# Performance work log

Hardware: AMD Instinct MI355X
Metric: run time of the kernel (lower is better)

Reference implementation:

```python
import jax, jax.numpy as jnp
import numpy as np

RANK = 16
ALPHA = 32
SCALING = ALPHA / RANK  # alpha / rank


def setup_inputs() -> dict:
    key = jax.random.key(0)
    k_x, k_w, k_b, k_a, k_bb = jax.random.split(key, 5)
    B, S, D_IN, D_OUT = 4, 2048, 4096, 4096
    x = jax.random.normal(k_x, (B, S, D_IN), dtype=jnp.float32)
    W = jax.random.normal(k_w, (D_OUT, D_IN), dtype=jnp.float32) * (1.0 / np.sqrt(D_IN))
    b = jax.random.normal(k_b, (D_OUT,), dtype=jnp.float32) * 0.02
    # LoRA init: A ~ N(0, 2/rank); B is zeros in the module, but we use small
    # random values so the adapter path is numerically exercised.
    lora_A = jax.random.normal(k_a, (RANK, D_IN), dtype=jnp.float32) * np.sqrt(2.0 / RANK)
    lora_B = jax.random.normal(k_bb, (D_OUT, RANK), dtype=jnp.float32) * 0.02
    return {"x": x, "W": W, "b": b, "lora_A": lora_A, "lora_B": lora_B}


def reference(x, W, b, lora_A, lora_B):
    # Base linear: x @ W^T + b
    base = jnp.einsum("bsd,od->bso", x, W) + b
    # LoRA path, fused as two rank-r matmuls (never materializing B@A):
    # (x @ A^T) @ B^T * scaling  ==  F.linear(x, B@A) * scaling
    xa = jnp.einsum("bsd,rd->bsr", x, lora_A)      # [B,S,r]
    lora = jnp.einsum("bsr,or->bso", xa, lora_B)    # [B,S,D_out]
    return base + lora * SCALING
```

## Files before the change

kernel.cpp:

```cpp
#include <hip/hip_runtime.h>
#include <hip/hip_bf16.h>

#define K_DIM 4096
#define N_DIM 4096
#define R_DIM 16
#define SCALING_F 2.0f

#define BM 256
#define BN 256
#define BK 64

typedef __attribute__((ext_vector_type(8))) short bf16x8;
typedef __attribute__((ext_vector_type(4))) float f32x4;

__device__ __forceinline__ ushort f2bf(float f) {
  union { float f; unsigned u; } v; v.f = f;
  unsigned u = v.u;
  u += 0x7FFF + ((u >> 16) & 1);
  return (ushort)(u >> 16);
}

__global__ void convert_x_kernel(const float* __restrict__ x,
                                 ushort* __restrict__ xb, long n4) {
  long i = (long)blockIdx.x * blockDim.x + threadIdx.x;
  long stride = (long)gridDim.x * blockDim.x;
  for (; i < n4; i += stride) {
    long idx = i * 4;
    float4 v = *(const float4*)(x + idx);
    ushort4 o;
    o.x = f2bf(v.x); o.y = f2bf(v.y); o.z = f2bf(v.z); o.w = f2bf(v.w);
    *(ushort4*)(xb + idx) = o;
  }
}

__global__ void fold_w_kernel(const float* __restrict__ W,
                              const float* __restrict__ A,
                              const float* __restrict__ Bl,
                              ushort* __restrict__ wb) {
  int o = blockIdx.x;
  float breg[R_DIM];
#pragma unroll
  for (int r = 0; r < R_DIM; ++r) breg[r] = Bl[o * R_DIM + r] * SCALING_F;
  for (int d0 = threadIdx.x * 4; d0 < K_DIM; d0 += blockDim.x * 4) {
    float4 w = *(const float4*)(W + (size_t)o * K_DIM + d0);
    float a0 = w.x, a1 = w.y, a2 = w.z, a3 = w.w;
#pragma unroll
    for (int r = 0; r < R_DIM; ++r) {
      float4 a = *(const float4*)(A + (size_t)r * K_DIM + d0);
      a0 += breg[r] * a.x; a1 += breg[r] * a.y;
      a2 += breg[r] * a.z; a3 += breg[r] * a.w;
    }
    ushort4 ob;
    ob.x = f2bf(a0); ob.y = f2bf(a1); ob.z = f2bf(a2); ob.w = f2bf(a3);
    *(ushort4*)(wb + (size_t)o * K_DIM + d0) = ob;
  }
}


#define RS 8192L

#define GLOAD(SRC, LOFF)                                                    \
  __builtin_amdgcn_global_load_lds(                                         \
      (const __attribute__((address_space(1))) void*)(SRC),                 \
      (__attribute__((address_space(3))) void*)(smem + (LOFF)), 16, 0, 0)

#define LDSA(BUF) ((BUF) * 32768)
#define LDSB(BUF) (65536 + (BUF) * 32768)

#define ST_A_EVEN(T, BUF) do {                                              \
    GLOAD(aS + (size_t)(T) * 128,            LDSA(BUF) + ldsDst);           \
    GLOAD(aS + (size_t)(T) * 128 + 128 * RS, LDSA(BUF) + 16384 + ldsDst); } while (0)
#define ST_A_ODD(T, BUF) do {                                               \
    GLOAD(aS + (size_t)(T) * 128 + 64 * RS,  LDSA(BUF) + 8192 + ldsDst);    \
    GLOAD(aS + (size_t)(T) * 128 + 192 * RS, LDSA(BUF) + 24576 + ldsDst); } while (0)
#define ST_B_H0(T, BUF) do {                                                \
    GLOAD(bS + (size_t)(T) * 128,            LDSB(BUF) + ldsDst);           \
    GLOAD(bS + (size_t)(T) * 128 + 64 * RS,  LDSB(BUF) + 8192 + ldsDst); } while (0)
#define ST_B_H1(T, BUF) do {                                                \
    GLOAD(bS + (size_t)(T) * 128 + 128 * RS, LDSB(BUF) + 16384 + ldsDst);   \
    GLOAD(bS + (size_t)(T) * 128 + 192 * RS, LDSB(BUF) + 24576 + ldsDst); } while (0)

#define LDA(M, CK, BUF) (*(const bf16x8*)(smem + LDSA(BUF) + aRd + (M) * 2048 + (CK)))
#define LDB(N, CK, BUF) (*(const bf16x8*)(smem + LDSB(BUF) + bRd + (N) * 2048 + (CK)))

#define MFMA16(MB, KK) do {                                                 \
    _Pragma("unroll") for (int mm = 0; mm < 4; ++mm)                        \
      _Pragma("unroll") for (int nn = 0; nn < 4; ++nn)                      \
        acc[(MB) + mm][nn] = __builtin_amdgcn_mfma_f32_16x16x32_bf16(       \
            afr[mm], bfr[nn][KK], acc[(MB) + mm][nn], 0, 0, 0); } while (0)

#define PH_OPEN()  __builtin_amdgcn_s_barrier(); __builtin_amdgcn_s_setprio(1)
#define PH_CLOSE() __builtin_amdgcn_s_setprio(0); __builtin_amdgcn_s_barrier()

__global__ __launch_bounds__(512, 2) void gemm_lora_kernel(
    const ushort* __restrict__ Ab, const ushort* __restrict__ Bb,
    const float* __restrict__ bias, float* __restrict__ C) {
  __shared__ char smem[131072];

  const int tid = threadIdx.x;
  const int wave = tid >> 6, lane = tid & 63;
  const int wm = wave >> 2, wn = wave & 3;
  const int fr = lane & 15, fq = lane >> 4;

  const int bid = blockIdx.x;
  const int bm = ((bid & 7) << 2) + ((bid >> 3) & 3);
  const int bn = bid >> 5;

  const int trow = tid >> 3;
  const int tswz = ((tid & 7) << 4) ^ ((trow & 7) << 4);
  const char* aS = (const char*)Ab + (size_t)(bm * BM + trow) * RS + tswz;
  const char* bS = (const char*)Bb + (size_t)(bn * BN + trow) * RS + tswz;
  const int ldsDst = tid << 4;

  const int sa  = (fr & 7) << 4;
  const int cK0 = (fq << 4) ^ sa;
  const int cK1 = (64 | (fq << 4)) ^ sa;
  const int aRd = ((wm << 7) + fr) << 7;
  const int bRd = ((wn << 6) + fr) << 7;

  f32x4 acc[8][4];
#pragma unroll
  for (int m = 0; m < 8; ++m)
#pragma unroll
    for (int n = 0; n < 4; ++n) acc[m][n] = (f32x4){0.f, 0.f, 0.f, 0.f};
  bf16x8 afr[4], bfr[4][2];

  ST_B_H0(0, 0); ST_B_H1(0, 0); ST_A_EVEN(0, 0); ST_A_ODD(0, 0);
  ST_B_H0(1, 1); ST_B_H1(1, 1); ST_A_EVEN(1, 1);
  asm volatile("s_waitcnt vmcnt(6)" ::: "memory");
  __builtin_amdgcn_s_barrier();

  const int NIT = K_DIM / (2 * BK);
#pragma unroll 1
  for (int i = 0; i < NIT; ++i) {
    const int t1 = 2 * i + 1, t2 = 2 * i + 2, t3 = 2 * i + 3;
    const bool last = (i == NIT - 1);

#pragma unroll
    for (int n = 0; n < 4; ++n) { bfr[n][0] = LDB(n, cK0, 0); bfr[n][1] = LDB(n, cK1, 0); }
#pragma unroll
    for (int m = 0; m < 4; ++m) afr[m] = LDA(m, cK0, 0);
    ST_A_ODD(t1, 1);
    PH_OPEN();  MFMA16(0, 0);  PH_CLOSE();

#pragma unroll
    for (int m = 0; m < 4; ++m) afr[m] = LDA(m, cK1, 0);
    if (!last) ST_B_H0(t2, 0);
    PH_OPEN();  MFMA16(0, 1);  PH_CLOSE();

#pragma unroll
    for (int m = 0; m < 4; ++m) afr[m] = LDA(m + 4, cK0, 0);
    if (!last) ST_B_H1(t2, 0);
    PH_OPEN();  MFMA16(4, 0);  PH_CLOSE();

#pragma unroll
    for (int m = 0; m < 4; ++m) afr[m] = LDA(m + 4, cK1, 0);
    if (!last) ST_A_EVEN(t2, 0);
    __builtin_amdgcn_s_barrier();
    __builtin_amdgcn_s_setprio(1);
    MFMA16(4, 1);
    __builtin_amdgcn_s_setprio(0);
    if (last) asm volatile("s_waitcnt vmcnt(0)" ::: "memory");
    else      asm volatile("s_waitcnt vmcnt(6)" ::: "memory");
    __builtin_amdgcn_s_barrier();

#pragma unroll
    for (int n = 0; n < 4; ++n) { bfr[n][0] = LDB(n, cK0, 1); bfr[n][1] = LDB(n, cK1, 1); }
#pragma unroll
    for (int m = 0; m < 4; ++m) afr[m] = LDA(m, cK0, 1);
    if (!last) ST_A_ODD(t2, 0);
    PH_OPEN();  MFMA16(0, 0);  PH_CLOSE();

#pragma unroll
    for (int m = 0; m < 4; ++m) afr[m] = LDA(m, cK1, 1);
    if (!last) ST_B_H0(t3, 1);
    PH_OPEN();  MFMA16(0, 1);  PH_CLOSE();

#pragma unroll
    for (int m = 0; m < 4; ++m) afr[m] = LDA(m + 4, cK0, 1);
    if (!last) ST_B_H1(t3, 1);
    PH_OPEN();  MFMA16(4, 0);  PH_CLOSE();

#pragma unroll
    for (int m = 0; m < 4; ++m) afr[m] = LDA(m + 4, cK1, 1);
    if (!last) ST_A_EVEN(t3, 1);
    __builtin_amdgcn_s_barrier();
    __builtin_amdgcn_s_setprio(1);
    MFMA16(4, 1);
    __builtin_amdgcn_s_setprio(0);
    if (!last) {
      asm volatile("s_waitcnt vmcnt(6)" ::: "memory");
      __builtin_amdgcn_s_barrier();
    }
  }

  const int ccol0 = bn * BN + wn * 64 + fr;
  float bv[4];
#pragma unroll
  for (int n = 0; n < 4; ++n) bv[n] = bias[ccol0 + n * 16];
  const int crow0 = bm * BM + wm * 128 + fq * 4;
#pragma unroll
  for (int m = 0; m < 8; ++m)
#pragma unroll
    for (int n = 0; n < 4; ++n)
#pragma unroll
      for (int v = 0; v < 4; ++v) {
        int row = crow0 + m * 16 + v;
        C[(size_t)row * N_DIM + ccol0 + n * 16] = acc[m][n][v] + bv[n];
      }
}

extern "C" void kernel_launch(void* const* d_in, const int* in_sizes, int n_in,
                              void* d_out, int out_size, void* d_ws, size_t ws_size,
                              hipStream_t stream) {
  const float* x  = (const float*)d_in[0];
  const float* W  = (const float*)d_in[1];
  const float* b  = (const float*)d_in[2];
  const float* lA = (const float*)d_in[3];
  const float* lB = (const float*)d_in[4];
  float* out = (float*)d_out;

  const int M = in_sizes[0] / K_DIM;

  ushort* xb = (ushort*)d_ws;
  ushort* wb = xb + (size_t)M * K_DIM;

  long n4 = (long)M * K_DIM / 4;
  convert_x_kernel<<<2048, 256, 0, stream>>>(x, xb, n4);
  fold_w_kernel<<<N_DIM, 256, 0, stream>>>(W, lA, lB, wb);
  gemm_lora_kernel<<<(M / BM) * (N_DIM / BN), 512, 0, stream>>>(xb, wb, b, out);
}
```

Measured before the change: 324.2 us.

## Switch GEMM to 32x32x16 MFMA tiles and merge prepass kernels

The main GEMM moves from 16x16x32 to 32x32x16 bf16 MFMA instructions. This changes the fragment layout, the LDS read addressing, the accumulator shape and the epilogue store pattern, and inserts explicit lgkmcnt waits between phases. The aim is fewer LDS fragment reads per FLOP and fewer MFMA issues. Separately, the x-conversion and W-folding kernels are merged into a single launch to save one launch and let both run concurrently. The larger accumulators may raise register pressure, and the new phase barriers add synchronization.

```diff
diff --git a/kernel.cpp b/kernel.cpp
--- a/kernel.cpp
+++ b/kernel.cpp
@@ -11,7 +11,7 @@
 #define BK 64
 
 typedef __attribute__((ext_vector_type(8))) short bf16x8;
-typedef __attribute__((ext_vector_type(4))) float f32x4;
+typedef __attribute__((ext_vector_type(16))) float f32x16;
 
 __device__ __forceinline__ ushort f2bf(float f) {
   union { float f; unsigned u; } v; v.f = f;
@@ -20,39 +20,38 @@
   return (ushort)(u >> 16);
 }
 
-__global__ void convert_x_kernel(const float* __restrict__ x,
-                                 ushort* __restrict__ xb, long n4) {
-  long i = (long)blockIdx.x * blockDim.x + threadIdx.x;
-  long stride = (long)gridDim.x * blockDim.x;
-  for (; i < n4; i += stride) {
-    long idx = i * 4;
-    float4 v = *(const float4*)(x + idx);
-    ushort4 o;
-    o.x = f2bf(v.x); o.y = f2bf(v.y); o.z = f2bf(v.z); o.w = f2bf(v.w);
-    *(ushort4*)(xb + idx) = o;
-  }
-}
-
-__global__ void fold_w_kernel(const float* __restrict__ W,
-                              const float* __restrict__ A,
-                              const float* __restrict__ Bl,
-                              ushort* __restrict__ wb) {
-  int o = blockIdx.x;
-  float breg[R_DIM];
-#pragma unroll
-  for (int r = 0; r < R_DIM; ++r) breg[r] = Bl[o * R_DIM + r] * SCALING_F;
-  for (int d0 = threadIdx.x * 4; d0 < K_DIM; d0 += blockDim.x * 4) {
-    float4 w = *(const float4*)(W + (size_t)o * K_DIM + d0);
-    float a0 = w.x, a1 = w.y, a2 = w.z, a3 = w.w;
-#pragma unroll
-    for (int r = 0; r < R_DIM; ++r) {
-      float4 a = *(const float4*)(A + (size_t)r * K_DIM + d0);
-      a0 += breg[r] * a.x; a1 += breg[r] * a.y;
-      a2 += breg[r] * a.z; a3 += breg[r] * a.w;
-    }
-    ushort4 ob;
-    ob.x = f2bf(a0); ob.y = f2bf(a1); ob.z = f2bf(a2); ob.w = f2bf(a3);
-    *(ushort4*)(wb + (size_t)o * K_DIM + d0) = ob;
+__global__ __launch_bounds__(256) void prepass_kernel(
+    const float* __restrict__ x, ushort* __restrict__ xb,
+    const float* __restrict__ W, const float* __restrict__ A,
+    const float* __restrict__ Bl, ushort* __restrict__ wb, long n4) {
+  if (blockIdx.x < N_DIM) {
+    int o = blockIdx.x;
+    float breg[R_DIM];
+#pragma unroll
+    for (int r = 0; r < R_DIM; ++r) breg[r] = Bl[o * R_DIM + r] * SCALING_F;
+    for (int d0 = threadIdx.x * 4; d0 < K_DIM; d0 += blockDim.x * 4) {
+      float4 w = *(const float4*)(W + (size_t)o * K_DIM + d0);
+      float a0 = w.x, a1 = w.y, a2 = w.z, a3 = w.w;
+#pragma unroll
+      for (int r = 0; r < R_DIM; ++r) {
+        float4 a = *(const float4*)(A + (size_t)r * K_DIM + d0);
+        a0 += breg[r] * a.x; a1 += breg[r] * a.y;
+        a2 += breg[r] * a.z; a3 += breg[r] * a.w;
+      }
+      ushort4 ob;
+      ob.x = f2bf(a0); ob.y = f2bf(a1); ob.z = f2bf(a2); ob.w = f2bf(a3);
+      *(ushort4*)(wb + (size_t)o * K_DIM + d0) = ob;
+    }
+  } else {
+    long i = (long)(blockIdx.x - N_DIM) * blockDim.x + threadIdx.x;
+    long stride = 2048L * blockDim.x;
+    for (; i < n4; i += stride) {
+      long idx = i * 4;
+      float4 v = *(const float4*)(x + idx);
+      ushort4 o;
+      o.x = f2bf(v.x); o.y = f2bf(v.y); o.z = f2bf(v.z); o.w = f2bf(v.w);
+      *(ushort4*)(xb + idx) = o;
+    }
   }
 }
 
@@ -80,17 +79,32 @@
     GLOAD(bS + (size_t)(T) * 128 + 128 * RS, LDSB(BUF) + 16384 + ldsDst);   \
     GLOAD(bS + (size_t)(T) * 128 + 192 * RS, LDSB(BUF) + 24576 + ldsDst); } while (0)
 
-#define LDA(M, CK, BUF) (*(const bf16x8*)(smem + LDSA(BUF) + aRd + (M) * 2048 + (CK)))
-#define LDB(N, CK, BUF) (*(const bf16x8*)(smem + LDSB(BUF) + bRd + (N) * 2048 + (CK)))
-
-#define MFMA16(MB, KK) do {                                                 \
-    _Pragma("unroll") for (int mm = 0; mm < 4; ++mm)                        \
-      _Pragma("unroll") for (int nn = 0; nn < 4; ++nn)                      \
-        acc[(MB) + mm][nn] = __builtin_amdgcn_mfma_f32_16x16x32_bf16(       \
-            afr[mm], bfr[nn][KK], acc[(MB) + mm][nn], 0, 0, 0); } while (0)
-
-#define PH_OPEN()  __builtin_amdgcn_s_barrier(); __builtin_amdgcn_s_setprio(1)
-#define PH_CLOSE() __builtin_amdgcn_s_setprio(0); __builtin_amdgcn_s_barrier()
+#define LDAx(MI, KS, BUF) (*(const bf16x8*)(smem + LDSA(BUF) + aRd + (MI) * 4096 + cs##KS))
+#define LDBx(NI, KS, BUF) (*(const bf16x8*)(smem + LDSB(BUF) + bRd + (NI) * 4096 + cs##KS))
+
+#define RDB_ALL(BUF) do {                                                   \
+    bfr[0][0] = LDBx(0, 0, BUF); bfr[0][1] = LDBx(0, 1, BUF);               \
+    bfr[0][2] = LDBx(0, 2, BUF); bfr[0][3] = LDBx(0, 3, BUF);               \
+    bfr[1][0] = LDBx(1, 0, BUF); bfr[1][1] = LDBx(1, 1, BUF);               \
+    bfr[1][2] = LDBx(1, 2, BUF); bfr[1][3] = LDBx(1, 3, BUF); } while (0)
+
+#define RDA(MB, K0, K1, BUF) do {                                           \
+    afr[0][0] = LDAx(MB, K0, BUF);       afr[0][1] = LDAx(MB, K1, BUF);     \
+    afr[1][0] = LDAx((MB) + 1, K0, BUF); afr[1][1] = LDAx((MB) + 1, K1, BUF); } while (0)
+
+#define MFMA8(MB, KH) do {                                                  \
+    _Pragma("unroll") for (int mm = 0; mm < 2; ++mm)                        \
+      _Pragma("unroll") for (int nn = 0; nn < 2; ++nn)                      \
+        _Pragma("unroll") for (int kk = 0; kk < 2; ++kk)                    \
+          acc[(MB) + mm][nn] = __builtin_amdgcn_mfma_f32_32x32x16_bf16(     \
+              afr[mm][kk], bfr[nn][2 * (KH) + kk], acc[(MB) + mm][nn], 0, 0, 0); } while (0)
+
+#define PH_MFMA(MB, KH) do {                                                \
+    __builtin_amdgcn_s_barrier();                                           \
+    asm volatile("s_waitcnt lgkmcnt(0)" ::: "memory");                      \
+    __builtin_amdgcn_s_setprio(1);                                          \
+    MFMA8(MB, KH);                                                          \
+    __builtin_amdgcn_s_setprio(0); } while (0)
 
 __global__ __launch_bounds__(512, 2) void gemm_lora_kernel(
     const ushort* __restrict__ Ab, const ushort* __restrict__ Bb,
@@ -100,7 +114,7 @@
   const int tid = threadIdx.x;
   const int wave = tid >> 6, lane = tid & 63;
   const int wm = wave >> 2, wn = wave & 3;
-  const int fr = lane & 15, fq = lane >> 4;
+  const int r31 = lane & 31, hi = lane >> 5;
 
   const int bid = blockIdx.x;
   const int bm = ((bid & 7) << 2) + ((bid >> 3) & 3);
@@ -112,18 +126,23 @@
   const char* bS = (const char*)Bb + (size_t)(bn * BN + trow) * RS + tswz;
   const int ldsDst = tid << 4;
 
-  const int sa  = (fr & 7) << 4;
-  const int cK0 = (fq << 4) ^ sa;
-  const int cK1 = (64 | (fq << 4)) ^ sa;
-  const int aRd = ((wm << 7) + fr) << 7;
-  const int bRd = ((wn << 6) + fr) << 7;
-
-  f32x4 acc[8][4];
-#pragma unroll
-  for (int m = 0; m < 8; ++m)
-#pragma unroll
-    for (int n = 0; n < 4; ++n) acc[m][n] = (f32x4){0.f, 0.f, 0.f, 0.f};
-  bf16x8 afr[4], bfr[4][2];
+  const int hi16 = hi << 4;
+  const int swz  = (lane & 7) << 4;
+  const int cs0 = (0  + hi16) ^ swz;
+  const int cs1 = (32 + hi16) ^ swz;
+  const int cs2 = (64 + hi16) ^ swz;
+  const int cs3 = (96 + hi16) ^ swz;
+  const int aRd = (wm * 128 + r31) * 128;
+  const int bRd = (wn * 64 + r31) * 128;
+
+  f32x16 acc[4][2];
+#pragma unroll
+  for (int m = 0; m < 4; ++m)
+#pragma unroll
+    for (int n = 0; n < 2; ++n)
+#pragma unroll
+      for (int v = 0; v < 16; ++v) acc[m][n][v] = 0.f;
+  bf16x8 afr[2][2], bfr[2][4];
 
   ST_B_H0(0, 0); ST_B_H1(0, 0); ST_A_EVEN(0, 0); ST_A_ODD(0, 0);
   ST_B_H0(1, 1); ST_B_H1(1, 1); ST_A_EVEN(1, 1);
@@ -136,78 +155,68 @@
     const int t1 = 2 * i + 1, t2 = 2 * i + 2, t3 = 2 * i + 3;
     const bool last = (i == NIT - 1);
 
-#pragma unroll
-    for (int n = 0; n < 4; ++n) { bfr[n][0] = LDB(n, cK0, 0); bfr[n][1] = LDB(n, cK1, 0); }
-#pragma unroll
-    for (int m = 0; m < 4; ++m) afr[m] = LDA(m, cK0, 0);
+    RDB_ALL(0);
+    RDA(0, 0, 1, 0);
     ST_A_ODD(t1, 1);
-    PH_OPEN();  MFMA16(0, 0);  PH_CLOSE();
-
-#pragma unroll
-    for (int m = 0; m < 4; ++m) afr[m] = LDA(m, cK1, 0);
+    asm volatile("s_waitcnt lgkmcnt(8)" ::: "memory");
+    PH_MFMA(0, 0);
+    __builtin_amdgcn_s_barrier();
+
+    RDA(0, 2, 3, 0);
     if (!last) ST_B_H0(t2, 0);
-    PH_OPEN();  MFMA16(0, 1);  PH_CLOSE();
-
-#pragma unroll
-    for (int m = 0; m < 4; ++m) afr[m] = LDA(m + 4, cK0, 0);
+    PH_MFMA(0, 1);
+    __builtin_amdgcn_s_barrier();
+
+    RDA(2, 0, 1, 0);
     if (!last) ST_B_H1(t2, 0);
-    PH_OPEN();  MFMA16(4, 0);  PH_CLOSE();
-
-#pragma unroll
-    for (int m = 0; m < 4; ++m) afr[m] = LDA(m + 4, cK1, 0);
+    PH_MFMA(2, 0);
+    __builtin_amdgcn_s_barrier();
+
+    RDA(2, 2, 3, 0);
     if (!last) ST_A_EVEN(t2, 0);
-    __builtin_amdgcn_s_barrier();
-    __builtin_amdgcn_s_setprio(1);
-    MFMA16(4, 1);
-    __builtin_amdgcn_s_setprio(0);
+    PH_MFMA(2, 1);
     if (last) asm volatile("s_waitcnt vmcnt(0)" ::: "memory");
     else      asm volatile("s_waitcnt vmcnt(6)" ::: "memory");
     __builtin_amdgcn_s_barrier();
 
-#pragma unroll
-    for (int n = 0; n < 4; ++n) { bfr[n][0] = LDB(n, cK0, 1); bfr[n][1] = LDB(n, cK1, 1); }
-#pragma unroll
-    for (int m = 0; m < 4; ++m) afr[m] = LDA(m, cK0, 1);
+    RDB_ALL(1);
+    RDA(0, 0, 1, 1);
     if (!last) ST_A_ODD(t2, 0);
-    PH_OPEN();  MFMA16(0, 0);  PH_CLOSE();
-
-#pragma unroll
-    for (int m = 0; m < 4; ++m) afr[m] = LDA(m, cK1, 1);
+    asm volatile("s_waitcnt lgkmcnt(8)" ::: "memory");
+    PH_MFMA(0, 0);
+    __builtin_amdgcn_s_barrier();
+
+    RDA(0, 2, 3, 1);
     if (!last) ST_B_H0(t3, 1);
-    PH_OPEN();  MFMA16(0, 1);  PH_CLOSE();
-
-#pragma unroll
-    for (int m = 0; m < 4; ++m) afr[m] = LDA(m + 4, cK0, 1);
+    PH_MFMA(0, 1);
+    __builtin_amdgcn_s_barrier();
+
+    RDA(2, 0, 1, 1);
     if (!last) ST_B_H1(t3, 1);
-    PH_OPEN();  MFMA16(4, 0);  PH_CLOSE();
-
-#pragma unroll
-    for (int m = 0; m < 4; ++m) afr[m] = LDA(m + 4, cK1, 1);
+    PH_MFMA(2, 0);
+    __builtin_amdgcn_s_barrier();
+
+    RDA(2, 2, 3, 1);
     if (!last) ST_A_EVEN(t3, 1);
-    __builtin_amdgcn_s_barrier();
-    __builtin_amdgcn_s_setprio(1);
-    MFMA16(4, 1);
-    __builtin_amdgcn_s_setprio(0);
+    PH_MFMA(2, 1);
     if (!last) {
       asm volatile("s_waitcnt vmcnt(6)" ::: "memory");
       __builtin_amdgcn_s_barrier();
     }
   }
 
-  const int ccol0 = bn * BN + wn * 64 + fr;
-  float bv[4];
-#pragma unroll
-  for (int n = 0; n < 4; ++n) bv[n] = bias[ccol0 + n * 16];
-  const int crow0 = bm * BM + wm * 128 + fq * 4;
-#pragma unroll
-  for (int m = 0; m < 8; ++m)
-#pragma unroll
-    for (int n = 0; n < 4; ++n)
-#pragma unroll
-      for (int v = 0; v < 4; ++v) {
-        int row = crow0 + m * 16 + v;
-        C[(size_t)row * N_DIM + ccol0 + n * 16] = acc[m][n][v] + bv[n];
-      }
+  const int ccol0 = bn * BN + wn * 64 + r31;
+  const float bv0 = bias[ccol0];
+  const float bv1 = bias[ccol0 + 32];
+  const int crow0 = bm * BM + wm * 128 + hi * 4;
+#pragma unroll
+  for (int mi = 0; mi < 4; ++mi)
+#pragma unroll
+    for (int v = 0; v < 16; ++v) {
+      int row = crow0 + mi * 32 + (v & 3) + 8 * (v >> 2);
+      C[(size_t)row * N_DIM + ccol0]      = acc[mi][0][v] + bv0;
+      C[(size_t)row * N_DIM + ccol0 + 32] = acc[mi][1][v] + bv1;
+    }
 }
 
 extern "C" void kernel_launch(void* const* d_in, const int* in_sizes, int n_in,
@@ -226,7 +235,6 @@
   ushort* wb = xb + (size_t)M * K_DIM;
 
   long n4 = (long)M * K_DIM / 4;
-  convert_x_kernel<<<2048, 256, 0, stream>>>(x, xb, n4);
-  fold_w_kernel<<<N_DIM, 256, 0, stream>>>(W, lA, lB, wb);
+  prepass_kernel<<<N_DIM + 2048, 256, 0, stream>>>(x, xb, W, lA, lB, wb, n4);
   gemm_lora_kernel<<<(M / BM) * (N_DIM / BN), 512, 0, stream>>>(xb, wb, b, out);
 }
```

Result: slower. 340.9 us (+5.2%).

## Merge prepass kernels and hand-schedule LDS reads with explicit waitcnts

Applied to the files above, without the earlier changes.

The x-conversion and W-folding kernels are merged into one launch, with block ranges split by blockIdx. This removes one launch and the serialization between the two prepasses. In the GEMM main loop, LDS fragment loads now go through inline-asm ds_read_b128 with explicit lgkmcnt waits and sched_barriers. This pins the order in which loads and MFMAs are issued, so the compiler cannot reorder them. Inline asm with volatile may block compiler optimizations and add waits that the compiler would otherwise avoid.

```diff
diff --git a/kernel.cpp b/kernel.cpp
--- a/kernel.cpp
+++ b/kernel.cpp
@@ -20,39 +20,44 @@
   return (ushort)(u >> 16);
 }
 
-__global__ void convert_x_kernel(const float* __restrict__ x,
-                                 ushort* __restrict__ xb, long n4) {
-  long i = (long)blockIdx.x * blockDim.x + threadIdx.x;
-  long stride = (long)gridDim.x * blockDim.x;
-  for (; i < n4; i += stride) {
-    long idx = i * 4;
-    float4 v = *(const float4*)(x + idx);
-    ushort4 o;
-    o.x = f2bf(v.x); o.y = f2bf(v.y); o.z = f2bf(v.z); o.w = f2bf(v.w);
-    *(ushort4*)(xb + idx) = o;
-  }
-}
-
-__global__ void fold_w_kernel(const float* __restrict__ W,
-                              const float* __restrict__ A,
-                              const float* __restrict__ Bl,
-                              ushort* __restrict__ wb) {
-  int o = blockIdx.x;
-  float breg[R_DIM];
-#pragma unroll
-  for (int r = 0; r < R_DIM; ++r) breg[r] = Bl[o * R_DIM + r] * SCALING_F;
-  for (int d0 = threadIdx.x * 4; d0 < K_DIM; d0 += blockDim.x * 4) {
-    float4 w = *(const float4*)(W + (size_t)o * K_DIM + d0);
-    float a0 = w.x, a1 = w.y, a2 = w.z, a3 = w.w;
-#pragma unroll
-    for (int r = 0; r < R_DIM; ++r) {
-      float4 a = *(const float4*)(A + (size_t)r * K_DIM + d0);
-      a0 += breg[r] * a.x; a1 += breg[r] * a.y;
-      a2 += breg[r] * a.z; a3 += breg[r] * a.w;
+__device__ __forceinline__ bf16x8 dsr128(unsigned addr) {
+  bf16x8 r;
+  asm volatile("ds_read_b128 %0, %1" : "=v"(r) : "v"(addr));
+  return r;
+}
+
+__global__ __launch_bounds__(256) void prepass_kernel(
+    const float* __restrict__ x, ushort* __restrict__ xb,
+    const float* __restrict__ W, const float* __restrict__ A,
+    const float* __restrict__ Bl, ushort* __restrict__ wb, long n4) {
+  if (blockIdx.x < N_DIM) {
+    int o = blockIdx.x;
+    float breg[R_DIM];
+#pragma unroll
+    for (int r = 0; r < R_DIM; ++r) breg[r] = Bl[o * R_DIM + r] * SCALING_F;
+    for (int d0 = threadIdx.x * 4; d0 < K_DIM; d0 += blockDim.x * 4) {
+      float4 w = *(const float4*)(W + (size_t)o * K_DIM + d0);
+      float a0 = w.x, a1 = w.y, a2 = w.z, a3 = w.w;
+#pragma unroll
+      for (int r = 0; r < R_DIM; ++r) {
+        float4 a = *(const float4*)(A + (size_t)r * K_DIM + d0);
+        a0 += breg[r] * a.x; a1 += breg[r] * a.y;
+        a2 += breg[r] * a.z; a3 += breg[r] * a.w;
+      }
+      ushort4 ob;
+      ob.x = f2bf(a0); ob.y = f2bf(a1); ob.z = f2bf(a2); ob.w = f2bf(a3);
+      *(ushort4*)(wb + (size_t)o * K_DIM + d0) = ob;
     }
-    ushort4 ob;
-    ob.x = f2bf(a0); ob.y = f2bf(a1); ob.z = f2bf(a2); ob.w = f2bf(a3);
-    *(ushort4*)(wb + (size_t)o * K_DIM + d0) = ob;
+  } else {
+    long i = (long)(blockIdx.x - N_DIM) * blockDim.x + threadIdx.x;
+    long stride = 2048L * blockDim.x;
+    for (; i < n4; i += stride) {
+      long idx = i * 4;
+      float4 v = *(const float4*)(x + idx);
+      ushort4 o;
+      o.x = f2bf(v.x); o.y = f2bf(v.y); o.z = f2bf(v.z); o.w = f2bf(v.w);
+      *(ushort4*)(xb + idx) = o;
+    }
   }
 }
 
@@ -80,8 +85,25 @@
     GLOAD(bS + (size_t)(T) * 128 + 128 * RS, LDSB(BUF) + 16384 + ldsDst);   \
     GLOAD(bS + (size_t)(T) * 128 + 192 * RS, LDSB(BUF) + 24576 + ldsDst); } while (0)
 
-#define LDA(M, CK, BUF) (*(const bf16x8*)(smem + LDSA(BUF) + aRd + (M) * 2048 + (CK)))
-#define LDB(N, CK, BUF) (*(const bf16x8*)(smem + LDSB(BUF) + bRd + (N) * 2048 + (CK)))
+#define READS_PH1(BUF) do {                                                 \
+    bfr[0][0] = dsr128(bLds[BUF] + 0 * 2048 + cK0);                         \
+    bfr[0][1] = dsr128(bLds[BUF] + 0 * 2048 + cK1);                         \
+    bfr[1][0] = dsr128(bLds[BUF] + 1 * 2048 + cK0);                         \
+    bfr[1][1] = dsr128(bLds[BUF] + 1 * 2048 + cK1);                         \
+    bfr[2][0] = dsr128(bLds[BUF] + 2 * 2048 + cK0);                         \
+    bfr[2][1] = dsr128(bLds[BUF] + 2 * 2048 + cK1);                         \
+    bfr[3][0] = dsr128(bLds[BUF] + 3 * 2048 + cK0);                         \
+    bfr[3][1] = dsr128(bLds[BUF] + 3 * 2048 + cK1);                         \
+    afr[0] = dsr128(aLds[BUF] + 0 * 2048 + cK0);                            \
+    afr[1] = dsr128(aLds[BUF] + 1 * 2048 + cK0);                            \
+    afr[2] = dsr128(aLds[BUF] + 2 * 2048 + cK0);                            \
+    afr[3] = dsr128(aLds[BUF] + 3 * 2048 + cK0); } while (0)
+
+#define READS_A(BUF, MB, CK) do {                                           \
+    afr[0] = dsr128(aLds[BUF] + ((MB) + 0) * 2048 + (CK));                  \
+    afr[1] = dsr128(aLds[BUF] + ((MB) + 1) * 2048 + (CK));                  \
+    afr[2] = dsr128(aLds[BUF] + ((MB) + 2) * 2048 + (CK));                  \
+    afr[3] = dsr128(aLds[BUF] + ((MB) + 3) * 2048 + (CK)); } while (0)
 
 #define MFMA16(MB, KK) do {                                                 \
     _Pragma("unroll") for (int mm = 0; mm < 4; ++mm)                        \
@@ -89,8 +111,14 @@
         acc[(MB) + mm][nn] = __builtin_amdgcn_mfma_f32_16x16x32_bf16(       \
             afr[mm], bfr[nn][KK], acc[(MB) + mm][nn], 0, 0, 0); } while (0)
 
-#define PH_OPEN()  __builtin_amdgcn_s_barrier(); __builtin_amdgcn_s_setprio(1)
-#define PH_CLOSE() __builtin_amdgcn_s_setprio(0); __builtin_amdgcn_s_barrier()
+#define PH_EXEC(MB, KK) do {                                                \
+    __builtin_amdgcn_s_barrier();                                           \
+    asm volatile("s_waitcnt lgkmcnt(0)" ::: "memory");                      \
+    __builtin_amdgcn_sched_barrier(0);                                      \
+    __builtin_amdgcn_s_setprio(1);                                          \
+    MFMA16(MB, KK);                                                         \
+    __builtin_amdgcn_s_setprio(0);                                          \
+    __builtin_amdgcn_s_barrier(); } while (0)
 
 __global__ __launch_bounds__(512, 2) void gemm_lora_kernel(
     const ushort* __restrict__ Ab, const ushort* __restrict__ Bb,
@@ -113,10 +141,14 @@
   const int ldsDst = tid << 4;
 
   const int sa  = (fr & 7) << 4;
-  const int cK0 = (fq << 4) ^ sa;
-  const int cK1 = (64 | (fq << 4)) ^ sa;
-  const int aRd = ((wm << 7) + fr) << 7;
-  const int bRd = ((wn << 6) + fr) << 7;
+  const unsigned cK0 = (unsigned)((fq << 4) ^ sa);
+  const unsigned cK1 = (unsigned)((64 | (fq << 4)) ^ sa);
+  const unsigned aRd = (unsigned)(((wm << 7) + fr) << 7);
+  const unsigned bRd = (unsigned)(((wn << 6) + fr) << 7);
+
+  const unsigned smemBase = (unsigned)(size_t)&smem[0];
+  const unsigned aLds[2] = {smemBase + LDSA(0) + aRd, smemBase + LDSA(1) + aRd};
+  const unsigned bLds[2] = {smemBase + LDSB(0) + bRd, smemBase + LDSB(1) + bRd};
 
   f32x4 acc[8][4];
 #pragma unroll
@@ -136,27 +168,24 @@
     const int t1 = 2 * i + 1, t2 = 2 * i + 2, t3 = 2 * i + 3;
     const bool last = (i == NIT - 1);
 
-#pragma unroll
-    for (int n = 0; n < 4; ++n) { bfr[n][0] = LDB(n, cK0, 0); bfr[n][1] = LDB(n, cK1, 0); }
-#pragma unroll
-    for (int m = 0; m < 4; ++m) afr[m] = LDA(m, cK0, 0);
+    READS_PH1(0);
     ST_A_ODD(t1, 1);
-    PH_OPEN();  MFMA16(0, 0);  PH_CLOSE();
-
-#pragma unroll
-    for (int m = 0; m < 4; ++m) afr[m] = LDA(m, cK1, 0);
+    asm volatile("s_waitcnt lgkmcnt(8)" ::: "memory");
+    PH_EXEC(0, 0);
+
+    READS_A(0, 0, cK1);
     if (!last) ST_B_H0(t2, 0);
-    PH_OPEN();  MFMA16(0, 1);  PH_CLOSE();
-
-#pragma unroll
-    for (int m = 0; m < 4; ++m) afr[m] = LDA(m + 4, cK0, 0);
+    PH_EXEC(0, 1);
+
+    READS_A(0, 4, cK0);
     if (!last) ST_B_H1(t2, 0);
-    PH_OPEN();  MFMA16(4, 0);  PH_CLOSE();
-
-#pragma unroll
-    for (int m = 0; m < 4; ++m) afr[m] = LDA(m + 4, cK1, 0);
+    PH_EXEC(4, 0);
+
+    READS_A(0, 4, cK1);
     if (!last) ST_A_EVEN(t2, 0);
     __builtin_amdgcn_s_barrier();
+    asm volatile("s_waitcnt lgkmcnt(0)" ::: "memory");
+    __builtin_amdgcn_sched_barrier(0);
     __builtin_amdgcn_s_setprio(1);
     MFMA16(4, 1);
     __builtin_amdgcn_s_setprio(0);
@@ -164,27 +193,24 @@
     else      asm volatile("s_waitcnt vmcnt(6)" ::: "memory");
     __builtin_amdgcn_s_barrier();
 
-#pragma unroll
-    for (int n = 0; n < 4; ++n) { bfr[n][0] = LDB(n, cK0, 1); bfr[n][1] = LDB(n, cK1, 1); }
-#pragma unroll
-    for (int m = 0; m < 4; ++m) afr[m] = LDA(m, cK0, 1);
+    READS_PH1(1);
     if (!last) ST_A_ODD(t2, 0);
-    PH_OPEN();  MFMA16(0, 0);  PH_CLOSE();
-
-#pragma unroll
-    for (int m = 0; m < 4; ++m) afr[m] = LDA(m, cK1, 1);
+    asm volatile("s_waitcnt lgkmcnt(8)" ::: "memory");
+    PH_EXEC(0, 0);
+
+    READS_A(1, 0, cK1);
     if (!last) ST_B_H0(t3, 1);
-    PH_OPEN();  MFMA16(0, 1);  PH_CLOSE();
-
-#pragma unroll
-    for (int m = 0; m < 4; ++m) afr[m] = LDA(m + 4, cK0, 1);
+    PH_EXEC(0, 1);
+
+    READS_A(1, 4, cK0);
     if (!last) ST_B_H1(t3, 1);
-    PH_OPEN();  MFMA16(4, 0);  PH_CLOSE();
-
-#pragma unroll
-    for (int m = 0; m < 4; ++m) afr[m] = LDA(m + 4, cK1, 1);
+    PH_EXEC(4, 0);
+
+    READS_A(1, 4, cK1);
     if (!last) ST_A_EVEN(t3, 1);
     __builtin_amdgcn_s_barrier();
+    asm volatile("s_waitcnt lgkmcnt(0)" ::: "memory");
+    __builtin_amdgcn_sched_barrier(0);
     __builtin_amdgcn_s_setprio(1);
     MFMA16(4, 1);
     __builtin_amdgcn_s_setprio(0);
@@ -226,7 +252,6 @@
   ushort* wb = xb + (size_t)M * K_DIM;
 
   long n4 = (long)M * K_DIM / 4;
-  convert_x_kernel<<<2048, 256, 0, stream>>>(x, xb, n4);
-  fold_w_kernel<<<N_DIM, 256, 0, stream>>>(W, lA, lB, wb);
+  prepass_kernel<<<N_DIM + 2048, 256, 0, stream>>>(x, xb, W, lA, lB, wb, n4);
   gemm_lora_kernel<<<(M / BM) * (N_DIM / BN), 512, 0, stream>>>(xb, wb, b, out);
 }
```

After: 491.1 us. +51.5%, slower.
